# Kernel optimization log

Measured on AMD Instinct MI355X. Metric: run time of the kernel, lower is better.

Reference implementation:

```python
import math
import jax, jax.numpy as jnp
import numpy as np

B, L, H, DH, DV = 4, 4096, 16, 128, 128
CHUNK = 1024
ROPE_BASE = 10000.0


def setup_inputs() -> dict:
    key = jax.random.key(0)
    k1, k2, k3 = jax.random.split(key, 3)
    q = jax.random.normal(k1, (B, L, H, DH), dtype=jnp.float32)
    k = jax.random.normal(k2, (B, L, H, DH), dtype=jnp.float32)
    v = jax.random.normal(k3, (B, L, H, DV), dtype=jnp.float32)
    return {"q": q, "k": k, "v": v}


def _apply_rope(q, k, start_index=0):
    # Faithful to RotaryEmbedding: complex rotate (x[..:half], x[half:..]) halves.
    T, D = q.shape[1], q.shape[-1]
    half = D // 2
    inv_freq = jnp.exp(jnp.arange(half, dtype=jnp.float32) * (-(math.log(ROPE_BASE) / half)))
    angles = (jnp.arange(T, dtype=jnp.float32) + start_index)[:, None] * inv_freq[None, :]  # (T, half)
    cos = jnp.cos(angles)[None, :, None, :]  # (1, T, 1, half)
    sin = jnp.sin(angles)[None, :, None, :]

    def rot(x):
        x1, x2 = x[..., :half], x[..., half:]
        return jnp.concatenate([x1 * cos - x2 * sin, x1 * sin + x2 * cos], axis=-1)

    return rot(q), rot(k)


def reference(q, k, v):
    # Training path: L > chunk_size, block-diagonal causal attention per chunk.
    q, k = _apply_rope(q, k, start_index=0)
    Bq, Lq, Hq, Dh = q.shape
    Dv = v.shape[-1]
    nc = Lq // CHUNK
    qc = q.reshape(Bq, nc, CHUNK, Hq, Dh)
    kc = k.reshape(Bq, nc, CHUNK, Hq, Dh)
    vc = v.reshape(Bq, nc, CHUNK, Hq, Dv)
    # scores: (B, nc, H, C, C)
    scores = jnp.einsum('bnihd,bnjhd->bnhij', qc, kc) / math.sqrt(Dh)
    i = jnp.arange(CHUNK)
    causal = jnp.where(i[:, None] >= i[None, :], 0.0, -jnp.inf).astype(jnp.float32)
    attn = jax.nn.softmax(scores.astype(jnp.float32) + causal, axis=-1).astype(q.dtype)
    out = jnp.einsum('bnhij,bnjhd->bnihd', attn, vc)  # (B, nc, C, H, Dv)
    return out.reshape(Bq, Lq, Hq * Dv)
```

## Files before the change

### kernel.cpp

```cpp
#include <hip/hip_runtime.h>
#include <math.h>

#define Bb   4
#define Ll   4096
#define Hh   16
#define DHd  128
#define DVd  128
#define CHk  1024
#define NCc  4

typedef __bf16 bf16x8 __attribute__((ext_vector_type(8)));
typedef float  f32x4  __attribute__((ext_vector_type(4)));

static __device__ __forceinline__ unsigned short f32_to_bf16(float f) {
  unsigned int u = __float_as_uint(f);
  u += 0x7FFFu + ((u >> 16) & 1u);
  return (unsigned short)(u >> 16);
}

#define GLDS16(src, dst) \
  __builtin_amdgcn_global_load_lds((const __attribute__((address_space(1))) void*)(src), \
                                   (__attribute__((address_space(3))) void*)(dst), 16, 0, 0)

__global__ void rope_table_k(float2* __restrict__ table) {
  int idx = blockIdx.x * 256 + threadIdx.x;
  if (idx >= Ll * 64) return;
  int l = idx >> 6, j = idx & 63;
  float inv_freq = expf((float)j * (-logf(10000.0f) / 64.0f));
  float ang = (float)l * inv_freq;
  float s, c;
  sincosf(ang, &s, &c);
  table[idx] = make_float2(c, s);
}

__global__ void rope_apply_k(const float4* __restrict__ q4, const float4* __restrict__ k4,
                             const float4* __restrict__ tb4,
                             ushort4* __restrict__ qr4, ushort4* __restrict__ kr4) {
  int idx = blockIdx.x * 256 + threadIdx.x;
  int j4 = idx & 15;
  int h  = (idx >> 4) & (Hh - 1);
  int l  = (idx >> 8) & (Ll - 1);
  int b  = idx >> 20;
  long base4 = ((long)((b * Ll + l) * Hh + h)) * 32;
  float4 cs0 = tb4[l * 32 + j4 * 2];
  float4 cs1 = tb4[l * 32 + j4 * 2 + 1];
  float4 a1 = q4[base4 + j4];
  float4 a2 = q4[base4 + 16 + j4];
  float4 b1 = k4[base4 + j4];
  float4 b2 = k4[base4 + 16 + j4];
  const float sc = 0.08838834764831845f;
  ushort4 o;
  o.x = f32_to_bf16((a1.x * cs0.x - a2.x * cs0.y) * sc);
  o.y = f32_to_bf16((a1.y * cs0.z - a2.y * cs0.w) * sc);
  o.z = f32_to_bf16((a1.z * cs1.x - a2.z * cs1.y) * sc);
  o.w = f32_to_bf16((a1.w * cs1.z - a2.w * cs1.w) * sc);
  qr4[base4 + j4] = o;
  o.x = f32_to_bf16((a1.x * cs0.y + a2.x * cs0.x) * sc);
  o.y = f32_to_bf16((a1.y * cs0.w + a2.y * cs0.z) * sc);
  o.z = f32_to_bf16((a1.z * cs1.y + a2.z * cs1.x) * sc);
  o.w = f32_to_bf16((a1.w * cs1.w + a2.w * cs1.z) * sc);
  qr4[base4 + 16 + j4] = o;
  o.x = f32_to_bf16(b1.x * cs0.x - b2.x * cs0.y);
  o.y = f32_to_bf16(b1.y * cs0.z - b2.y * cs0.w);
  o.z = f32_to_bf16(b1.z * cs1.x - b2.z * cs1.y);
  o.w = f32_to_bf16(b1.w * cs1.z - b2.w * cs1.w);
  kr4[base4 + j4] = o;
  o.x = f32_to_bf16(b1.x * cs0.y + b2.x * cs0.x);
  o.y = f32_to_bf16(b1.y * cs0.w + b2.y * cs0.z);
  o.z = f32_to_bf16(b1.z * cs1.y + b2.z * cs1.x);
  o.w = f32_to_bf16(b1.w * cs1.w + b2.w * cs1.z);
  kr4[base4 + 16 + j4] = o;
}

__global__ void vtrans_k(const float4* __restrict__ v4, unsigned short* __restrict__ vt) {
  int bid = blockIdx.x;
  int kb = bid & 15;
  int h  = (bid >> 4) & 15;
  int n  = (bid >> 8) & 3;
  int b  = bid >> 10;
  __shared__ __align__(16) unsigned short tile[DVd][68];
  int tid = threadIdx.x;
#pragma unroll
  for (int it = 0; it < 8; ++it) {
    int i4 = it * 256 + tid;
    int r  = i4 >> 5;
    int c4 = i4 & 31;
    float4 val = v4[((long)((b * Ll + n * CHk + kb * 64 + r) * Hh + h)) * 32 + c4];
    tile[c4 * 4 + 0][r] = f32_to_bf16(val.x);
    tile[c4 * 4 + 1][r] = f32_to_bf16(val.y);
    tile[c4 * 4 + 2][r] = f32_to_bf16(val.z);
    tile[c4 * 4 + 3][r] = f32_to_bf16(val.w);
  }
  __syncthreads();
  long ob = ((long)((b * NCc + n) * Hh + h)) * (DVd * CHk) + kb * 64;
#pragma unroll
  for (int it = 0; it < 8; ++it) {
    int i4 = it * 256 + tid;
    int dv  = i4 >> 4;
    int k4i = i4 & 15;
    ushort4 o = *(const ushort4*)&tile[dv][k4i * 4];
    *(ushort4*)&vt[ob + (long)dv * CHk + k4i * 4] = o;
  }
}

__device__ __forceinline__ void stage_kv(const unsigned short* krb, const unsigned short* vtb,
                                         unsigned short* Kb, unsigned short* Vb,
                                         int kvb, int tid) {
  int wbase = tid & 192;
#pragma unroll
  for (int i = 0; i < 4; ++i) {
    int t = i * 256 + tid;
    int row = t >> 4;
    int c16 = (t & 15) ^ ((t >> 4) & 7);
    const char* src = (const char*)(krb + (long)(kvb + row) * (Hh * DHd)) + c16 * 16;
    char* dst = (char*)Kb + (i * 256 + wbase) * 16;
    GLDS16(src, dst);
  }
#pragma unroll
  for (int i = 0; i < 4; ++i) {
    int t = i * 256 + tid;
    int row = t >> 3;
    int c16 = (t & 7) ^ ((t >> 3) & 7);
    const char* src = (const char*)(vtb + (long)row * CHk + kvb) + c16 * 16;
    char* dst = (char*)Vb + (i * 256 + wbase) * 16;
    GLDS16(src, dst);
  }
}

__global__ __launch_bounds__(256, 2)
void attn_k(const unsigned short* __restrict__ qr,
            const unsigned short* __restrict__ kr,
            const unsigned short* __restrict__ vt,
            float* __restrict__ out) {
  __shared__ __align__(16) unsigned short Klds[2][64 * 128];
  __shared__ __align__(16) unsigned short Vlds[2][128 * 64];
  __shared__ __align__(16) unsigned short plds[4][16][72];

  int bid = blockIdx.x;
  int qt = 15 - (bid & 15);
  int h  = (bid >> 4) & 15;
  int n  = (bid >> 8) & 3;
  int b  = bid >> 10;
  int tid  = threadIdx.x;
  int wid  = tid >> 6;
  int lane = tid & 63;
  int lg = lane >> 4;
  int lc = lane & 15;

  const unsigned short* krb = kr + ((long)((b * Ll + n * CHk) * Hh + h)) * DHd;
  const unsigned short* vtb = vt + ((long)((b * NCc + n) * Hh + h)) * (DVd * CHk);

  int qrow0 = qt * 64 + wid * 16;
  const unsigned short* qrow =
      qr + ((long)((b * Ll + n * CHk + qrow0 + lc) * Hh + h)) * DHd;
  bf16x8 qf[4];
#pragma unroll
  for (int ks = 0; ks < 4; ++ks)
    qf[ks] = *reinterpret_cast<const bf16x8*>(qrow + ks * 32 + lg * 8);

  f32x4 oacc[8];
#pragma unroll
  for (int i = 0; i < 8; ++i) oacc[i] = (f32x4){0.f, 0.f, 0.f, 0.f};
  float mrow[4], lrow[4];
#pragma unroll
  for (int r = 0; r < 4; ++r) { mrow[r] = -3.0e38f; lrow[r] = 0.f; }

  stage_kv(krb, vtb, &Klds[0][0], &Vlds[0][0], 0, tid);
  __syncthreads();

  int cur = 0;
  int swz = (lc & 7) << 4;
  for (int kvt = 0; kvt <= qt; ++kvt) {
    int kvb = kvt * 64;
    if (kvt < qt)
      stage_kv(krb, vtb, &Klds[cur ^ 1][0], &Vlds[cur ^ 1][0], kvb + 64, tid);

    const char* Kb = (const char*)&Klds[cur][0];
    f32x4 sacc[4];
#pragma unroll
    for (int ct = 0; ct < 4; ++ct) sacc[ct] = (f32x4){0.f, 0.f, 0.f, 0.f};
#pragma unroll
    for (int ct = 0; ct < 4; ++ct) {
      int rowb = (ct * 16 + lc) * 256;
#pragma unroll
      for (int ks = 0; ks < 4; ++ks) {
        bf16x8 kf = *(const bf16x8*)(Kb + rowb + ((ks * 64 + lg * 16) ^ swz));
        sacc[ct] = __builtin_amdgcn_mfma_f32_16x16x32_bf16(qf[ks], kf, sacc[ct], 0, 0, 0);
      }
    }

    float p[4][4];
#pragma unroll
    for (int ct = 0; ct < 4; ++ct)
#pragma unroll
      for (int r = 0; r < 4; ++r) p[ct][r] = sacc[ct][r];
    if (kvt == qt) {
#pragma unroll
      for (int ct = 0; ct < 4; ++ct) {
        int col = kvb + ct * 16 + lc;
#pragma unroll
        for (int r = 0; r < 4; ++r)
          if (col > qrow0 + lg * 4 + r) p[ct][r] = -3.0e38f;
      }
    }
#pragma unroll
    for (int r = 0; r < 4; ++r) {
      float tmax = fmaxf(fmaxf(p[0][r], p[1][r]), fmaxf(p[2][r], p[3][r]));
      tmax = fmaxf(tmax, __shfl_xor(tmax, 1));
      tmax = fmaxf(tmax, __shfl_xor(tmax, 2));
      tmax = fmaxf(tmax, __shfl_xor(tmax, 4));
      tmax = fmaxf(tmax, __shfl_xor(tmax, 8));
      float mnew = fmaxf(mrow[r], tmax);
      float corr = __expf(mrow[r] - mnew);
      mrow[r] = mnew;
      float ps = 0.f;
#pragma unroll
      for (int ct = 0; ct < 4; ++ct) {
        p[ct][r] = __expf(p[ct][r] - mnew);
        ps += p[ct][r];
      }
      ps += __shfl_xor(ps, 1);
      ps += __shfl_xor(ps, 2);
      ps += __shfl_xor(ps, 4);
      ps += __shfl_xor(ps, 8);
      lrow[r] = lrow[r] * corr + ps;
#pragma unroll
      for (int dt = 0; dt < 8; ++dt) oacc[dt][r] *= corr;
    }

#pragma unroll
    for (int ct = 0; ct < 4; ++ct)
#pragma unroll
      for (int r = 0; r < 4; ++r)
        plds[wid][lg * 4 + r][ct * 16 + lc] = f32_to_bf16(p[ct][r]);
    const char* Pb = (const char*)&plds[wid][0][0];
    bf16x8 pf0 = *(const bf16x8*)(Pb + lc * 144 + lg * 16);
    bf16x8 pf1 = *(const bf16x8*)(Pb + lc * 144 + 64 + lg * 16);

    const char* Vb = (const char*)&Vlds[cur][0];
#pragma unroll
    for (int dt = 0; dt < 8; ++dt) {
      int rowb = (dt * 16 + lc) * 128;
      bf16x8 vf0 = *(const bf16x8*)(Vb + rowb + ((lg * 16) ^ swz));
      bf16x8 vf1 = *(const bf16x8*)(Vb + rowb + ((64 + lg * 16) ^ swz));
      oacc[dt] = __builtin_amdgcn_mfma_f32_16x16x32_bf16(pf0, vf0, oacc[dt], 0, 0, 0);
      oacc[dt] = __builtin_amdgcn_mfma_f32_16x16x32_bf16(pf1, vf1, oacc[dt], 0, 0, 0);
    }

    __syncthreads();
    cur ^= 1;
  }

  long ob = (long)(b * Ll + n * CHk + qrow0 + lg * 4) * (Hh * DVd) + h * DVd + lc;
#pragma unroll
  for (int r = 0; r < 4; ++r) {
    float invl = 1.0f / lrow[r];
#pragma unroll
    for (int dt = 0; dt < 8; ++dt)
      out[ob + (long)r * (Hh * DVd) + dt * 16] = oacc[dt][r] * invl;
  }
}

extern "C" void kernel_launch(void* const* d_in, const int* in_sizes, int n_in,
                              void* d_out, int out_size, void* d_ws, size_t ws_size,
                              hipStream_t stream) {
  const float* q = (const float*)d_in[0];
  const float* k = (const float*)d_in[1];
  const float* v = (const float*)d_in[2];
  float* out = (float*)d_out;

  char* ws = (char*)d_ws;
  float2* table = (float2*)ws;
  unsigned short* qrw = (unsigned short*)(ws + (2l << 20));
  unsigned short* krw = qrw + (long)Bb * Ll * Hh * DHd;
  unsigned short* vtw = krw + (long)Bb * Ll * Hh * DHd;

  hipLaunchKernelGGL(rope_table_k, dim3((Ll * 64) / 256), dim3(256), 0, stream, table);
  hipLaunchKernelGGL(rope_apply_k, dim3((Bb * Ll * Hh * 16) / 256), dim3(256), 0, stream,
                     (const float4*)q, (const float4*)k, (const float4*)table,
                     (ushort4*)qrw, (ushort4*)krw);
  hipLaunchKernelGGL(vtrans_k, dim3(Bb * NCc * Hh * 16), dim3(256), 0, stream,
                     (const float4*)v, vtw);
  hipLaunchKernelGGL(attn_k, dim3(Bb * NCc * Hh * 16), dim3(256), 0, stream,
                     qrw, krw, vtw, out);
}
```

Before: 733.4 us.

## Fuse RoPE and V transpose; stage KV through registers with single LDS buffer

Merges the RoPE-apply and V-transpose kernels into one preprocessing kernel, removing a launch. The attention kernel drops the async global-to-LDS double buffer in favour of register prefetch of the next KV tile into a single LDS buffer, and raises launch-bounds occupancy from 2 to 3 blocks. The goal is higher occupancy through less LDS per block. The cost is extra register pressure and a second barrier per iteration.

New measurement: 1.071 ms. 1.46x slower.

```diff
diff --git a/kernel.cpp b/kernel.cpp
--- a/kernel.cpp
+++ b/kernel.cpp
@@ -17,10 +17,6 @@
   u += 0x7FFFu + ((u >> 16) & 1u);
   return (unsigned short)(u >> 16);
 }
-
-#define GLDS16(src, dst) \
-  __builtin_amdgcn_global_load_lds((const __attribute__((address_space(1))) void*)(src), \
-                                   (__attribute__((address_space(3))) void*)(dst), 16, 0, 0)
 
 __global__ void rope_table_k(float2* __restrict__ table) {
   int idx = blockIdx.x * 256 + threadIdx.x;
@@ -33,59 +29,62 @@
   table[idx] = make_float2(c, s);
 }
 
-__global__ void rope_apply_k(const float4* __restrict__ q4, const float4* __restrict__ k4,
-                             const float4* __restrict__ tb4,
-                             ushort4* __restrict__ qr4, ushort4* __restrict__ kr4) {
-  int idx = blockIdx.x * 256 + threadIdx.x;
-  int j4 = idx & 15;
-  int h  = (idx >> 4) & (Hh - 1);
-  int l  = (idx >> 8) & (Ll - 1);
-  int b  = idx >> 20;
-  long base4 = ((long)((b * Ll + l) * Hh + h)) * 32;
-  float4 cs0 = tb4[l * 32 + j4 * 2];
-  float4 cs1 = tb4[l * 32 + j4 * 2 + 1];
-  float4 a1 = q4[base4 + j4];
-  float4 a2 = q4[base4 + 16 + j4];
-  float4 b1 = k4[base4 + j4];
-  float4 b2 = k4[base4 + 16 + j4];
-  const float sc = 0.08838834764831845f;
-  ushort4 o;
-  o.x = f32_to_bf16((a1.x * cs0.x - a2.x * cs0.y) * sc);
-  o.y = f32_to_bf16((a1.y * cs0.z - a2.y * cs0.w) * sc);
-  o.z = f32_to_bf16((a1.z * cs1.x - a2.z * cs1.y) * sc);
-  o.w = f32_to_bf16((a1.w * cs1.z - a2.w * cs1.w) * sc);
-  qr4[base4 + j4] = o;
-  o.x = f32_to_bf16((a1.x * cs0.y + a2.x * cs0.x) * sc);
-  o.y = f32_to_bf16((a1.y * cs0.w + a2.y * cs0.z) * sc);
-  o.z = f32_to_bf16((a1.z * cs1.y + a2.z * cs1.x) * sc);
-  o.w = f32_to_bf16((a1.w * cs1.w + a2.w * cs1.z) * sc);
-  qr4[base4 + 16 + j4] = o;
-  o.x = f32_to_bf16(b1.x * cs0.x - b2.x * cs0.y);
-  o.y = f32_to_bf16(b1.y * cs0.z - b2.y * cs0.w);
-  o.z = f32_to_bf16(b1.z * cs1.x - b2.z * cs1.y);
-  o.w = f32_to_bf16(b1.w * cs1.z - b2.w * cs1.w);
-  kr4[base4 + j4] = o;
-  o.x = f32_to_bf16(b1.x * cs0.y + b2.x * cs0.x);
-  o.y = f32_to_bf16(b1.y * cs0.w + b2.y * cs0.z);
-  o.z = f32_to_bf16(b1.z * cs1.y + b2.z * cs1.x);
-  o.w = f32_to_bf16(b1.w * cs1.w + b2.w * cs1.z);
-  kr4[base4 + 16 + j4] = o;
-}
-
-__global__ void vtrans_k(const float4* __restrict__ v4, unsigned short* __restrict__ vt) {
+__global__ void pre_k(const float4* __restrict__ q4, const float4* __restrict__ k4,
+                      const float4* __restrict__ v4, const float4* __restrict__ tb4,
+                      ushort4* __restrict__ qr4, ushort4* __restrict__ kr4,
+                      unsigned short* __restrict__ vt) {
   int bid = blockIdx.x;
   int kb = bid & 15;
   int h  = (bid >> 4) & 15;
   int n  = (bid >> 8) & 3;
   int b  = bid >> 10;
+  int tid = threadIdx.x;
+  int l0 = n * CHk + kb * 64;
+
+#pragma unroll
+  for (int it = 0; it < 4; ++it) {
+    int w  = it * 256 + tid;
+    int j4 = w & 15;
+    int r  = w >> 4;
+    int l  = l0 + r;
+    long base4 = ((long)((b * Ll + l) * Hh + h)) * 32;
+    float4 cs0 = tb4[(long)l * 32 + j4 * 2];
+    float4 cs1 = tb4[(long)l * 32 + j4 * 2 + 1];
+    float4 a1 = q4[base4 + j4];
+    float4 a2 = q4[base4 + 16 + j4];
+    float4 b1 = k4[base4 + j4];
+    float4 b2 = k4[base4 + 16 + j4];
+    const float sc = 0.08838834764831845f;
+    ushort4 o;
+    o.x = f32_to_bf16((a1.x * cs0.x - a2.x * cs0.y) * sc);
+    o.y = f32_to_bf16((a1.y * cs0.z - a2.y * cs0.w) * sc);
+    o.z = f32_to_bf16((a1.z * cs1.x - a2.z * cs1.y) * sc);
+    o.w = f32_to_bf16((a1.w * cs1.z - a2.w * cs1.w) * sc);
+    qr4[base4 + j4] = o;
+    o.x = f32_to_bf16((a1.x * cs0.y + a2.x * cs0.x) * sc);
+    o.y = f32_to_bf16((a1.y * cs0.w + a2.y * cs0.z) * sc);
+    o.z = f32_to_bf16((a1.z * cs1.y + a2.z * cs1.x) * sc);
+    o.w = f32_to_bf16((a1.w * cs1.w + a2.w * cs1.z) * sc);
+    qr4[base4 + 16 + j4] = o;
+    o.x = f32_to_bf16(b1.x * cs0.x - b2.x * cs0.y);
+    o.y = f32_to_bf16(b1.y * cs0.z - b2.y * cs0.w);
+    o.z = f32_to_bf16(b1.z * cs1.x - b2.z * cs1.y);
+    o.w = f32_to_bf16(b1.w * cs1.z - b2.w * cs1.w);
+    kr4[base4 + j4] = o;
+    o.x = f32_to_bf16(b1.x * cs0.y + b2.x * cs0.x);
+    o.y = f32_to_bf16(b1.y * cs0.w + b2.y * cs0.z);
+    o.z = f32_to_bf16(b1.z * cs1.y + b2.z * cs1.x);
+    o.w = f32_to_bf16(b1.w * cs1.w + b2.w * cs1.z);
+    kr4[base4 + 16 + j4] = o;
+  }
+
   __shared__ __align__(16) unsigned short tile[DVd][68];
-  int tid = threadIdx.x;
 #pragma unroll
   for (int it = 0; it < 8; ++it) {
     int i4 = it * 256 + tid;
     int r  = i4 >> 5;
     int c4 = i4 & 31;
-    float4 val = v4[((long)((b * Ll + n * CHk + kb * 64 + r) * Hh + h)) * 32 + c4];
+    float4 val = v4[((long)((b * Ll + l0 + r) * Hh + h)) * 32 + c4];
     tile[c4 * 4 + 0][r] = f32_to_bf16(val.x);
     tile[c4 * 4 + 1][r] = f32_to_bf16(val.y);
     tile[c4 * 4 + 2][r] = f32_to_bf16(val.z);
@@ -103,37 +102,47 @@
   }
 }
 
-__device__ __forceinline__ void stage_kv(const unsigned short* krb, const unsigned short* vtb,
-                                         unsigned short* Kb, unsigned short* Vb,
-                                         int kvb, int tid) {
-  int wbase = tid & 192;
-#pragma unroll
-  for (int i = 0; i < 4; ++i) {
-    int t = i * 256 + tid;
-    int row = t >> 4;
-    int c16 = (t & 15) ^ ((t >> 4) & 7);
-    const char* src = (const char*)(krb + (long)(kvb + row) * (Hh * DHd)) + c16 * 16;
-    char* dst = (char*)Kb + (i * 256 + wbase) * 16;
-    GLDS16(src, dst);
-  }
-#pragma unroll
-  for (int i = 0; i < 4; ++i) {
-    int t = i * 256 + tid;
-    int row = t >> 3;
-    int c16 = (t & 7) ^ ((t >> 3) & 7);
-    const char* src = (const char*)(vtb + (long)row * CHk + kvb) + c16 * 16;
-    char* dst = (char*)Vb + (i * 256 + wbase) * 16;
-    GLDS16(src, dst);
-  }
-}
-
-__global__ __launch_bounds__(256, 2)
+__device__ __forceinline__ void stage_load(const unsigned short* krb,
+                                           const unsigned short* vtb,
+                                           int kvb, int tid,
+                                           float4* kreg, float4* vreg) {
+#pragma unroll
+  for (int i = 0; i < 4; ++i) {
+    int t = i * 256 + tid;
+    kreg[i] = *(const float4*)((const char*)(krb + (long)(kvb + (t >> 4)) * (Hh * DHd)) +
+                               (t & 15) * 16);
+  }
+#pragma unroll
+  for (int i = 0; i < 4; ++i) {
+    int t = i * 256 + tid;
+    vreg[i] = *(const float4*)((const char*)(vtb + (long)(t >> 3) * CHk + kvb) +
+                               (t & 7) * 16);
+  }
+}
+
+__device__ __forceinline__ void stage_write(unsigned short* Kb, unsigned short* Vb,
+                                            int tid, const float4* kreg, const float4* vreg) {
+#pragma unroll
+  for (int i = 0; i < 4; ++i) {
+    int t = i * 256 + tid;
+    int row = t >> 4, c = (t & 15) ^ (row & 7);
+    *(float4*)((char*)Kb + row * 256 + c * 16) = kreg[i];
+  }
+#pragma unroll
+  for (int i = 0; i < 4; ++i) {
+    int t = i * 256 + tid;
+    int row = t >> 3, c = (t & 7) ^ (row & 7);
+    *(float4*)((char*)Vb + row * 128 + c * 16) = vreg[i];
+  }
+}
+
+__global__ __launch_bounds__(256, 3)
 void attn_k(const unsigned short* __restrict__ qr,
             const unsigned short* __restrict__ kr,
             const unsigned short* __restrict__ vt,
             float* __restrict__ out) {
-  __shared__ __align__(16) unsigned short Klds[2][64 * 128];
-  __shared__ __align__(16) unsigned short Vlds[2][128 * 64];
+  __shared__ __align__(16) unsigned short Klds[64 * 128];
+  __shared__ __align__(16) unsigned short Vlds[128 * 64];
   __shared__ __align__(16) unsigned short plds[4][16][72];
 
   int bid = blockIdx.x;
@@ -165,17 +174,17 @@
 #pragma unroll
   for (int r = 0; r < 4; ++r) { mrow[r] = -3.0e38f; lrow[r] = 0.f; }
 
-  stage_kv(krb, vtb, &Klds[0][0], &Vlds[0][0], 0, tid);
+  float4 kreg[4], vreg[4];
+  stage_load(krb, vtb, 0, tid, kreg, vreg);
+  stage_write(Klds, Vlds, tid, kreg, vreg);
+  if (qt > 0) stage_load(krb, vtb, 64, tid, kreg, vreg);
   __syncthreads();
 
-  int cur = 0;
   int swz = (lc & 7) << 4;
   for (int kvt = 0; kvt <= qt; ++kvt) {
     int kvb = kvt * 64;
-    if (kvt < qt)
-      stage_kv(krb, vtb, &Klds[cur ^ 1][0], &Vlds[cur ^ 1][0], kvb + 64, tid);
-
-    const char* Kb = (const char*)&Klds[cur][0];
+
+    const char* Kb = (const char*)&Klds[0];
     f32x4 sacc[4];
 #pragma unroll
     for (int ct = 0; ct < 4; ++ct) sacc[ct] = (f32x4){0.f, 0.f, 0.f, 0.f};
@@ -237,7 +246,7 @@
     bf16x8 pf0 = *(const bf16x8*)(Pb + lc * 144 + lg * 16);
     bf16x8 pf1 = *(const bf16x8*)(Pb + lc * 144 + 64 + lg * 16);
 
-    const char* Vb = (const char*)&Vlds[cur][0];
+    const char* Vb = (const char*)&Vlds[0];
 #pragma unroll
     for (int dt = 0; dt < 8; ++dt) {
       int rowb = (dt * 16 + lc) * 128;
@@ -247,8 +256,12 @@
       oacc[dt] = __builtin_amdgcn_mfma_f32_16x16x32_bf16(pf1, vf1, oacc[dt], 0, 0, 0);
     }
 
-    __syncthreads();
-    cur ^= 1;
+    if (kvt < qt) {
+      __syncthreads();
+      stage_write(Klds, Vlds, tid, kreg, vreg);
+      if (kvt + 1 < qt) stage_load(krb, vtb, kvb + 128, tid, kreg, vreg);
+      __syncthreads();
+    }
   }
 
   long ob = (long)(b * Ll + n * CHk + qrow0 + lg * 4) * (Hh * DVd) + h * DVd + lc;
@@ -276,11 +289,9 @@
   unsigned short* vtw = krw + (long)Bb * Ll * Hh * DHd;
 
   hipLaunchKernelGGL(rope_table_k, dim3((Ll * 64) / 256), dim3(256), 0, stream, table);
-  hipLaunchKernelGGL(rope_apply_k, dim3((Bb * Ll * Hh * 16) / 256), dim3(256), 0, stream,
-                     (const float4*)q, (const float4*)k, (const float4*)table,
-                     (ushort4*)qrw, (ushort4*)krw);
-  hipLaunchKernelGGL(vtrans_k, dim3(Bb * NCc * Hh * 16), dim3(256), 0, stream,
-                     (const float4*)v, vtw);
+  hipLaunchKernelGGL(pre_k, dim3(Bb * NCc * Hh * 16), dim3(256), 0, stream,
+                     (const float4*)q, (const float4*)k, (const float4*)v,
+                     (const float4*)table, (ushort4*)qrw, (ushort4*)krw, vtw);
   hipLaunchKernelGGL(attn_k, dim3(Bb * NCc * Hh * 16), dim3(256), 0, stream,
                      qrw, krw, vtw, out);
 }
```
